# Performance work log

Measured on AMD Instinct MI355X. Metric: run time of the kernel, lower is better.

Reference implementation:

```python
import jax, jax.numpy as jnp
import numpy as np

N = 1024          # num_features
H = N // 2        # core dimension (num_params // 2)
NB = 4            # num_blocks
B = 16384         # batch


def _lifted_core(rot_params, diag_params):
    """Build the (N, N) lifted core matrix for one Cayley block."""
    # skew-symmetric matrix from the H rotation params
    S = rot_params[:, None] - rot_params[None, :]            # (H, H)
    I = jnp.eye(H, dtype=rot_params.dtype)
    rotation = jnp.linalg.solve(I - S, I + S)                # Cayley transform
    core = diag_params[:, None] * rotation                   # diag(d) @ rotation
    # rot90(core, k=o) only depends on o mod 4 -> precompute 4 variants
    rots = jnp.stack([core,
                      jnp.rot90(core, 1),
                      jnp.rot90(core, 2),
                      jnp.rot90(core, 3)])                   # (4, H, H)

    def body(lifted, o):
        blk = jax.lax.dynamic_slice(lifted, (o, o), (H, H)) + rots[o % 4]
        return jax.lax.dynamic_update_slice(lifted, blk, (o, o)), None

    lifted, _ = jax.lax.scan(body, jnp.zeros((N, N), dtype=core.dtype),
                             jnp.arange(H + 1))
    return lifted


def setup_inputs() -> dict:
    key = jax.random.key(0)
    ks = jax.random.split(key, 5)
    x = jax.random.normal(ks[0], (B, N), dtype=jnp.float32)
    enc_rot = jax.random.normal(ks[1], (NB, H), dtype=jnp.float32)
    enc_diag = jax.random.normal(ks[2], (NB, H), dtype=jnp.float32)
    dec_rot = jax.random.normal(ks[3], (NB, H), dtype=jnp.float32)
    dec_diag = jax.random.normal(ks[4], (NB, H), dtype=jnp.float32)
    return {"x": x, "enc_rot": enc_rot, "enc_diag": enc_diag,
            "dec_rot": dec_rot, "dec_diag": dec_diag}


def reference(x, enc_rot, enc_diag, dec_rot, dec_diag):
    s = x
    for i in range(NB):                                      # encoder blocks
        s = s @ _lifted_core(enc_rot[i], enc_diag[i]).T
    bottleneck = s
    out = s
    for i in range(NB):                                      # decoder blocks
        out = out @ _lifted_core(dec_rot[i], dec_diag[i]).T
    return bottleneck, out
```

## Files before the change

### kernel.cpp

```cpp
#include <hip/hip_runtime.h>
#include <hip/hip_bf16.h>
#include <cstdint>
#include <cstddef>

#define H 512
#define NFEAT 1024
#define BATCH 16384
#define LM ((size_t)1 << 20)
#define KOP 576

using bf16 = __hip_bfloat16;
using bf16x8 = __attribute__((ext_vector_type(8))) __bf16;
using f32x4 = __attribute__((ext_vector_type(4))) float;
using f32x16 = __attribute__((ext_vector_type(16))) float;

__device__ __forceinline__ void gload16(void* lds, const void* g) {
  __builtin_amdgcn_global_load_lds(
      (__attribute__((address_space(1))) void*)g,
      (__attribute__((address_space(3))) void*)lds,
      16, 0, 0);
}

__global__ void prep_kernel(const float* __restrict__ er, const float* __restrict__ ed,
                            const float* __restrict__ dr, const float* __restrict__ dd,
                            float* __restrict__ ab) {
  const int mat = blockIdx.x;
  const int lane = threadIdx.x;
  const float* u = (mat < 4) ? (er + mat * H) : (dr + (mat - 4) * H);
  const float* d = (mat < 4) ? (ed + mat * H) : (dd + (mat - 4) * H);

  double s = 0.0, q = 0.0;
  for (int k = 0; k < 8; ++k) {
    double v = (double)u[lane + 64 * k];
    s += v;
    q += v * v;
  }
  for (int off = 32; off; off >>= 1) {
    s += __shfl_down(s, off);
    q += __shfl_down(q, off);
  }
  s = __shfl(s, 0);
  q = __shfl(q, 0);

  const double det = 1.0 - s * s + (double)H * q;
  const double cuv = 2.0 * (1.0 + s) / det;
  const double cuu = -2.0 * (double)H / det;
  const double cvv = -2.0 * q / det;
  const double cvu = -2.0 * (1.0 - s) / det;

  float* a = ab + mat * 1024;
  float* b = a + H;
  for (int k = 0; k < 8; ++k) {
    int idx = lane + 64 * k;
    double ui = (double)u[idx], di = (double)d[idx];
    a[idx] = (float)(di * (cuv * ui + cvv));
    b[idx] = (float)(di * (cuu * ui + cvu));
  }
}

__global__ __launch_bounds__(256) void prep2_kernel(
    const float* __restrict__ er, const float* __restrict__ ed,
    const float* __restrict__ dr, const float* __restrict__ dd,
    const float* __restrict__ ab, float* __restrict__ Tpref) {
  __shared__ float buf[4][512];
  __shared__ float tmp[4][512];
  const int mat = blockIdx.x;
  const float* d = (mat < 4) ? (ed + mat * H) : (dd + (mat - 4) * H);
  const float* a = ab + mat * 1024;
  const int t = threadIdx.x;
  for (int m = t; m < 512; m += 256) {
    buf[0][m] = a[m];
    buf[1][m] = a[511 - m];
    buf[2][m] = d[m];
    buf[3][m] = d[511 - m];
  }
  __syncthreads();
  for (int s = 4; s <= 256; s <<= 1) {
    for (int m = t; m < 512; m += 256)
#pragma unroll
      for (int q = 0; q < 4; ++q) tmp[q][m] = (m >= s) ? buf[q][m - s] : 0.f;
    __syncthreads();
    for (int m = t; m < 512; m += 256)
#pragma unroll
      for (int q = 0; q < 4; ++q) buf[q][m] += tmp[q][m];
    __syncthreads();
  }
  float* tp = Tpref + mat * 2048;
  for (int m = t; m < 512; m += 256) {
    tp[m] = buf[0][m];
    tp[512 + m] = buf[1][m];
    tp[1024 + m] = buf[2][m];
    tp[1536 + m] = buf[3][m];
  }
}

__global__ __launch_bounds__(256) void genops_kernel(
    const float* __restrict__ er, const float* __restrict__ dr,
    const float* __restrict__ ab,
    bf16* __restrict__ Ah, bf16* __restrict__ Al,
    bf16* __restrict__ Bh, bf16* __restrict__ Bl) {
  const int x = blockIdx.x;
  const int mat = blockIdx.y;
  const float* u = (mat < 4) ? (er + mat * H) : (dr + (mat - 4) * H);
  const float* b = ab + mat * 1024 + H;
  const int t = threadIdx.x;
  const size_t base = ((size_t)mat * 1024 + x) * KOP;
  for (int k = t; k < KOP; k += 256) {
    float av = 0.f, bv = 0.f;
    if (k <= 128) {
      const int o = 4 * k;
      const int ia = x - o;
      av = (ia >= 0 && ia < 512) ? b[ia] : 0.f;
      bv = (ia >= 0 && ia < 512) ? u[ia] : 0.f;
    } else if (k <= 256) {
      const int o = 4 * (k - 129) + 1;
      const int ia = 511 - x + o;
      const int ib = x - o;
      av = (ia >= 0 && ia < 512) ? u[ia] : 0.f;
      bv = (ib >= 0 && ib < 512) ? b[ib] : 0.f;
    } else if (k <= 384) {
      const int o = 4 * (k - 257) + 2;
      const int ia = 511 - x + o;
      av = (ia >= 0 && ia < 512) ? b[ia] : 0.f;
      bv = (ia >= 0 && ia < 512) ? u[ia] : 0.f;
    } else if (k <= 512) {
      const int o = 4 * (k - 385) + 3;
      const int ia = x - o;
      const int ib = 511 - x + o;
      av = (ia >= 0 && ia < 512) ? u[ia] : 0.f;
      bv = (ib >= 0 && ib < 512) ? b[ib] : 0.f;
    }
    const bf16 ah = __float2bfloat16(av);
    Ah[base + k] = ah;
    Al[base + k] = __float2bfloat16(av - __bfloat162float(ah));
    const bf16 bh = __float2bfloat16(bv);
    Bh[base + k] = bh;
    Bl[base + k] = __float2bfloat16(bv - __bfloat162float(bh));
  }
}

__global__ __launch_bounds__(256) void buildgemm_kernel(
    const bf16* __restrict__ Ah, const bf16* __restrict__ Al,
    const bf16* __restrict__ Bh, const bf16* __restrict__ Bl,
    const float* __restrict__ ed, const float* __restrict__ dd,
    const float* __restrict__ Tpref, bf16* __restrict__ Lbase) {
  __shared__ __align__(16) bf16 smem[4 * 8192];
  __shared__ float pa[512], parev[512], pd[512], pdrev[512], sdl[512];
  bf16* sAh = smem;
  bf16* sAl = smem + 8192;
  bf16* sBh = smem + 16384;
  bf16* sBl = smem + 24576;

  const int tid = threadIdx.x;
  const int lane = tid & 63;
  const int wave = tid >> 6;
  const int wr = wave >> 1;
  const int wc = wave & 1;
  const int mat = blockIdx.z;
  const int row0 = blockIdx.x * 128;
  const int col0 = blockIdx.y * 128;

  {
    const float* tp = Tpref + mat * 2048;
    const float* d = (mat < 4) ? (ed + mat * H) : (dd + (mat - 4) * H);
    for (int m = tid; m < 512; m += 256) {
      pa[m] = tp[m];
      parev[m] = tp[512 + m];
      pd[m] = tp[1024 + m];
      pdrev[m] = tp[1536 + m];
      sdl[m] = d[m];
    }
  }

  const size_t OPS = (size_t)mat * 1024 * KOP;
  const int srow = tid >> 3;
  const int sce = (((tid * 16) ^ (((tid >> 3) & 7) << 4)) & 127) >> 1;
  const size_t abase = OPS + (size_t)(row0 + srow) * KOP + sce;
  const size_t bbase = OPS + (size_t)(col0 + srow) * KOP + sce;
  const int dst0 = tid * 8;

  f32x16 acc[2][2] = {};

  for (int kt = 0; kt < 9; ++kt) {
    const int k0 = kt * 64;
#pragma unroll
    for (int q = 0; q < 4; ++q) {
      const size_t ga = abase + (size_t)(32 * q) * KOP + k0;
      const size_t gb = bbase + (size_t)(32 * q) * KOP + k0;
      const int dq = q * 2048 + dst0;
      gload16(sAh + dq, Ah + ga);
      gload16(sAl + dq, Al + ga);
      gload16(sBh + dq, Bh + gb);
      gload16(sBl + dq, Bl + gb);
    }
    __syncthreads();

    const int l31 = lane & 31;
    const int kh16 = (lane >> 5) * 16;
#pragma unroll
    for (int ks = 0; ks < 4; ++ks) {
      bf16x8 fah[2], fal[2], fbh[2], fbl[2];
#pragma unroll
      for (int m = 0; m < 2; ++m) {
        const int arow = wr * 64 + m * 32 + l31;
        const int abk = (arow * 128 + ks * 32 + kh16) ^ ((arow & 7) << 4);
        fah[m] = *(const bf16x8*)((const char*)sAh + abk);
        fal[m] = *(const bf16x8*)((const char*)sAl + abk);
        const int brow = wc * 64 + m * 32 + l31;
        const int bbk = (brow * 128 + ks * 32 + kh16) ^ ((brow & 7) << 4);
        fbh[m] = *(const bf16x8*)((const char*)sBh + bbk);
        fbl[m] = *(const bf16x8*)((const char*)sBl + bbk);
      }
#pragma unroll
      for (int m = 0; m < 2; ++m)
#pragma unroll
        for (int n = 0; n < 2; ++n) {
          acc[m][n] = __builtin_amdgcn_mfma_f32_32x32x16_bf16(fah[m], fbh[n], acc[m][n], 0, 0, 0);
          acc[m][n] = __builtin_amdgcn_mfma_f32_32x32x16_bf16(fah[m], fbl[n], acc[m][n], 0, 0, 0);
          acc[m][n] = __builtin_amdgcn_mfma_f32_32x32x16_bf16(fal[m], fbh[n], acc[m][n], 0, 0, 0);
        }
    }
    __syncthreads();
  }

  auto apart = [&](int i, int j) -> float {
    const int lo = max(0, max(i, j) - 511);
    const int hi = min(512, min(i, j));
    if (lo > hi) return 0.f;
    float v = 0.f;
    {
      int o1 = lo + ((0 - lo) & 3), o2 = hi - (hi & 3);
      if (o1 <= o2) { int mx = i - o1, mn = i - o2; v += pa[mx] - (mn >= 4 ? pa[mn - 4] : 0.f); }
    }
    {
      int o1 = lo + ((1 - lo) & 3), o2 = hi - ((hi - 1) & 3);
      if (o1 <= o2) { int mx = j - o1, mn = j - o2; v += pa[mx] - (mn >= 4 ? pa[mn - 4] : 0.f); }
    }
    {
      int o1 = lo + ((2 - lo) & 3), o2 = hi - ((hi - 2) & 3);
      if (o1 <= o2) { int mx = i - o1, mn = i - o2; v += parev[mx] - (mn >= 4 ? parev[mn - 4] : 0.f); }
    }
    {
      int o1 = lo + ((3 - lo) & 3), o2 = hi - ((hi - 3) & 3);
      if (o1 <= o2) { int mx = j - o1, mn = j - o2; v += parev[mx] - (mn >= 4 ? parev[mn - 4] : 0.f); }
    }
    if (i == j) {
      {
        int o1 = lo + ((0 - lo) & 3), o2 = hi - (hi & 3);
        if (o1 <= o2) { int mx = i - o1, mn = i - o2; v += pd[mx] - (mn >= 4 ? pd[mn - 4] : 0.f); }
      }
      {
        int o1 = lo + ((2 - lo) & 3), o2 = hi - ((hi - 2) & 3);
        if (o1 <= o2) { int mx = i - o1, mn = i - o2; v += pdrev[mx] - (mn >= 4 ? pdrev[mn - 4] : 0.f); }
      }
    }
    const int m2 = i + j - 511;
    if (m2 >= 0 && !(m2 & 1)) {
      const int os = m2 >> 1;
      if (os >= lo && os <= hi) {
        const int r = os & 3;
        if (r == 1) v += sdl[j - os];
        else if (r == 3) v += sdl[511 - (j - os)];
      }
    }
    return v;
  };

  const int ocol0 = col0 + wc * 64 + (lane & 31);
  const int rb = (lane >> 5) << 2;
#pragma unroll
  for (int m = 0; m < 2; ++m)
#pragma unroll
    for (int n = 0; n < 2; ++n)
#pragma unroll
      for (int r = 0; r < 16; ++r) {
        const int grow = row0 + wr * 64 + m * 32 + (r & 3) + ((r >> 2) << 3) + rb;
        const int gcol = ocol0 + n * 32;
        const float v = acc[m][n][r] + apart(grow, gcol);
        const size_t off = ((size_t)mat << 21) + ((size_t)grow << 10) + (size_t)gcol;
        const bf16 hb = __float2bfloat16(v);
        Lbase[off] = hb;
        Lbase[off + LM] = __float2bfloat16(v - __bfloat162float(hb));
      }
}

__global__ void splith_kernel(const float* __restrict__ x, bf16* __restrict__ h) {
  const int n4 = BATCH * NFEAT / 4;
  int idx = blockIdx.x * blockDim.x + threadIdx.x;
  int stride = gridDim.x * blockDim.x;
  for (int i = idx; i < n4; i += stride) {
    float4 v = ((const float4*)x)[i];
    union { bf16 b[4]; short4 s; } Hu;
    Hu.b[0] = __float2bfloat16(v.x);
    Hu.b[1] = __float2bfloat16(v.y);
    Hu.b[2] = __float2bfloat16(v.z);
    Hu.b[3] = __float2bfloat16(v.w);
    ((short4*)h)[i] = Hu.s;
  }
}

struct TPtrs { const bf16* s; bf16* d; };
struct T6 { TPtrs t[6]; };

__global__ __launch_bounds__(256) void transposeB_kernel(T6 p) {
  const bf16* S = p.t[blockIdx.z].s;
  bf16* D = p.t[blockIdx.z].d;
  __shared__ ushort tile[64][68];
  const int i0 = blockIdx.x * 64, j0 = blockIdx.y * 64;
  const int tid = threadIdx.x;
  const int rr = tid >> 4;
  const int cc = (tid & 15) * 4;
#pragma unroll
  for (int it = 0; it < 4; ++it) {
    const int row = it * 16 + rr;
    const size_t so = (size_t)(i0 + row) * 1024 + j0 + cc;
    ushort4 v = *(const ushort4*)((const ushort*)S + so);
    tile[row][cc] = v.x; tile[row][cc + 1] = v.y;
    tile[row][cc + 2] = v.z; tile[row][cc + 3] = v.w;
  }
  __syncthreads();
#pragma unroll
  for (int it = 0; it < 4; ++it) {
    const int row = it * 16 + rr;
    ushort4 o;
    o.x = tile[cc][row];     o.y = tile[cc + 1][row];
    o.z = tile[cc + 2][row]; o.w = tile[cc + 3][row];
    const size_t dofs = (size_t)(j0 + row) * 1024 + i0 + cc;
    *(ushort4*)((ushort*)D + dofs) = o;
  }
}

struct GPtrs { const bf16* a; const bf16* b; bf16* yh; bf16* yl; };
struct G4 { GPtrs g[4]; };

__global__ __launch_bounds__(256) void chaingemm4_kernel(G4 p) {
  GPtrs q = p.g[blockIdx.z];
  const bf16* A = q.a;
  const bf16* Bh = q.b;
  const bf16* Bl = q.b + LM;

  __shared__ __align__(16) bf16 smem[2 * 3 * 4096];

  const int tid = threadIdx.x;
  const int lane = tid & 63;
  const int wave = tid >> 6;
  const int wr = wave >> 1, wc = wave & 1;
  const int r0 = blockIdx.x * 64, c0 = blockIdx.y * 64;

  const int srow = tid >> 3;
  const int scol = (((tid & 7) ^ (srow & 7))) * 8;
  const int dst = tid * 8;
  const size_t ga0 = (size_t)(r0 + srow) * 1024 + scol;
  const size_t gb0 = (size_t)(c0 + srow) * 1024 + scol;

  auto STAGE = [&](int nb, int k0) {
    bf16* base = smem + nb * 12288;
    gload16(base + dst,        A + ga0 + k0);
    gload16(base + 2048 + dst, A + ga0 + 32 * 1024 + k0);
    gload16(base + 4096 + dst,        Bh + gb0 + k0);
    gload16(base + 4096 + 2048 + dst, Bh + gb0 + 32 * 1024 + k0);
    gload16(base + 8192 + dst,        Bl + gb0 + k0);
    gload16(base + 8192 + 2048 + dst, Bl + gb0 + 32 * 1024 + k0);
  };

  const int l31 = lane & 31;
  const int klg = lane >> 5;
  const int ar = wr * 32 + l31;
  const int br = wc * 32 + l31;
  int aoff[4], boff[4];
#pragma unroll
  for (int ks = 0; ks < 4; ++ks) {
    const int lgA = (ks << 1) | klg;
    aoff[ks] = ar * 64 + ((lgA ^ (ar & 7)) << 3);
    boff[ks] = br * 64 + ((lgA ^ (br & 7)) << 3);
  }

  f32x16 acc = {};

  STAGE(0, 0);
  asm volatile("s_waitcnt vmcnt(0)" ::: "memory");
  __builtin_amdgcn_s_barrier();

  for (int t = 0; t < 16; ++t) {
    const int buf = t & 1;
    const int nb = buf ^ 1;
    const bool pf = (t < 15);
    if (pf) STAGE(nb, (t + 1) * 64);

    const bf16* pA = smem + buf * 12288;
    const bf16* pBh = pA + 4096;
    const bf16* pBl = pA + 8192;
#pragma unroll
    for (int ks = 0; ks < 4; ++ks) {
      bf16x8 ah = *(const bf16x8*)(pA + aoff[ks]);
      bf16x8 bh = *(const bf16x8*)(pBh + boff[ks]);
      bf16x8 bl = *(const bf16x8*)(pBl + boff[ks]);
      acc = __builtin_amdgcn_mfma_f32_32x32x16_bf16(ah, bh, acc, 0, 0, 0);
      acc = __builtin_amdgcn_mfma_f32_32x32x16_bf16(ah, bl, acc, 0, 0, 0);
    }
    if (pf) asm volatile("s_waitcnt vmcnt(0)" ::: "memory");
    __builtin_amdgcn_s_barrier();
  }

  const int oc = c0 + wc * 32 + l31;
  const int rb = (lane >> 5) << 2;
#pragma unroll
  for (int r = 0; r < 16; ++r) {
    const int gr = r0 + wr * 32 + (r & 3) + ((r >> 2) << 3) + rb;
    const size_t off = (size_t)gr * 1024 + oc;
    const float v = acc[r];
    const bf16 hb = __float2bfloat16(v);
    q.yh[off] = hb;
    q.yl[off] = __float2bfloat16(v - __bfloat162float(hb));
  }
}

__global__ __launch_bounds__(256, 2) void gemmbig_kernel(
    const bf16* __restrict__ A, const bf16* __restrict__ Bh_,
    float* __restrict__ Y0, float* __restrict__ Y1) {
  __shared__ __align__(16) bf16 smem[3 * 12288];

  const int tid = threadIdx.x;
  const int lane = tid & 63;
  const int wave = tid >> 6;
  const int wr = wave >> 1;
  const int wc = wave & 1;

  const int pdisp = blockIdx.x;
  const int xcd = pdisp & 7;
  const int chk = pdisp >> 3;
  const int row0 = (xcd * 16 + (chk >> 3)) * 128;
  const int col0 = (chk & 7) * 256;

  const int sr = tid >> 2;
  const int sc = ((tid & 3) ^ ((tid >> 3) & 3)) * 8;
  const size_t abase0 = (size_t)(row0 + sr) * NFEAT + sc;
  const size_t abase1 = abase0 + (size_t)64 * NFEAT;
  const size_t bbase = (size_t)(col0 + sr) * NFEAT + sc;
  const int dst = tid * 8;

  auto STAGE_A = [&](int buf, int k0) {
    bf16* base = smem + buf * 12288;
    gload16(base + dst, A + abase0 + k0);
    gload16(base + 2048 + dst, A + abase1 + k0);
  };
  auto STAGE_B = [&](int buf, int k0) {
    bf16* base = smem + buf * 12288 + 4096;
#pragma unroll
    for (int q = 0; q < 4; ++q)
      gload16(base + q * 2048 + dst, Bh_ + bbase + (size_t)(64 * q) * NFEAT + k0);
  };

  const int l15 = lane & 15;
  const int kcol = ((lane >> 4) * 16) ^ (((l15 >> 1) & 3) << 4);
  int aoff[4], boff[8];
#pragma unroll
  for (int fr = 0; fr < 4; ++fr)
    aoff[fr] = (wr * 64 + fr * 16 + l15) * 64 + kcol;
#pragma unroll
  for (int fc = 0; fc < 8; ++fc)
    boff[fc] = 8192 + (wc * 128 + fc * 16 + l15) * 64 + kcol;

  auto LD = [&](int buf, int off) {
    return *(const bf16x8*)((const char*)(smem + buf * 12288) + off);
  };

  f32x4 acc[4][8] = {};

  STAGE_A(0, 0); STAGE_B(0, 0);
  STAGE_A(1, 32); STAGE_B(1, 32);
  asm volatile("s_waitcnt vmcnt(6)" ::: "memory");
  __builtin_amdgcn_s_barrier();

  for (int T = 0; T < 32; ++T) {
    const int buf = T % 3;
    if (T < 30) {
      const int nb = (T + 2) % 3;
      STAGE_A(nb, (T + 2) * 32);
      STAGE_B(nb, (T + 2) * 32);
    }

    bf16x8 fa[4], fb[4];
#pragma unroll
    for (int fr = 0; fr < 4; ++fr) fa[fr] = LD(buf, aoff[fr]);
#pragma unroll
    for (int fc = 0; fc < 4; ++fc) fb[fc] = LD(buf, boff[fc]);
    __builtin_amdgcn_s_setprio(1);
#pragma unroll
    for (int fr = 0; fr < 4; ++fr)
#pragma unroll
      for (int fc = 0; fc < 4; ++fc)
        acc[fr][fc] = __builtin_amdgcn_mfma_f32_16x16x32_bf16(fa[fr], fb[fc], acc[fr][fc], 0, 0, 0);
    __builtin_amdgcn_s_setprio(0);
#pragma unroll
    for (int fc = 0; fc < 4; ++fc) fb[fc] = LD(buf, boff[4 + fc]);
    __builtin_amdgcn_s_setprio(1);
#pragma unroll
    for (int fr = 0; fr < 4; ++fr)
#pragma unroll
      for (int fc = 0; fc < 4; ++fc)
        acc[fr][4 + fc] = __builtin_amdgcn_mfma_f32_16x16x32_bf16(fa[fr], fb[fc], acc[fr][4 + fc], 0, 0, 0);
    __builtin_amdgcn_s_setprio(0);

    if (T <= 29) {
      asm volatile("s_waitcnt vmcnt(6)" ::: "memory");
    } else if (T == 30) {
      asm volatile("s_waitcnt vmcnt(0)" ::: "memory");
    }
    __builtin_amdgcn_s_barrier();
  }

  float* Yb = (col0 < 1024) ? Y0 : (Y1 - 1024);
  const int orow = row0 + wr * 64 + (lane >> 4) * 4;
  const int ocol = col0 + wc * 128 + l15;
#pragma unroll
  for (int fr = 0; fr < 4; ++fr)
#pragma unroll
    for (int fc = 0; fc < 8; ++fc)
#pragma unroll
      for (int r = 0; r < 4; ++r) {
        const int grow = orow + fr * 16 + r;
        const int gcol = ocol + fc * 16;
        Yb[(size_t)grow * NFEAT + (size_t)gcol] = acc[fr][fc][r];
      }
}

extern "C" void kernel_launch(void* const* d_in, const int* in_sizes, int n_in,
                              void* d_out, int out_size, void* d_ws, size_t ws_size,
                              hipStream_t stream) {
  (void)in_sizes; (void)n_in; (void)out_size; (void)ws_size;
  const float* x  = (const float*)d_in[0];
  const float* er = (const float*)d_in[1];
  const float* ed = (const float*)d_in[2];
  const float* dr = (const float*)d_in[3];
  const float* dd = (const float*)d_in[4];

  float* O0 = (float*)d_out;
  float* O1 = O0 + (size_t)BATCH * NFEAT;

  bf16* Lb = (bf16*)d_ws;
  float* ab = (float*)(Lb + 16 * LM);
  bf16* Qh = (bf16*)(ab + 8 * 1024);

  float* Tpref = O0;
  bf16* SB = (bf16*)((char*)O0 + (1 << 20));
  auto slot = [&](int s) { return SB + (size_t)s * LM; };

  const size_t OPN = (size_t)8 * 1024 * KOP;
  bf16* Aoph = (bf16*)O1;
  bf16* Aopl = Aoph + OPN;
  bf16* Boph = Aopl + OPN;
  bf16* Bopl = Boph + OPN;

  prep_kernel<<<8, 64, 0, stream>>>(er, ed, dr, dd, ab);
  prep2_kernel<<<8, 256, 0, stream>>>(er, ed, dr, dd, ab, Tpref);
  genops_kernel<<<dim3(1024, 8), 256, 0, stream>>>(er, dr, ab, Aoph, Aopl, Boph, Bopl);
  buildgemm_kernel<<<dim3(8, 8, 8), 256, 0, stream>>>(Aoph, Aopl, Boph, Bopl,
                                                      ed, dd, Tpref, Lb);
  splith_kernel<<<4096, 256, 0, stream>>>(x, Qh);

  {
    T6 p;
    p.t[0] = {Lb + 0 * LM,  slot(0)};
    p.t[1] = {Lb + 4 * LM,  slot(2)};
    p.t[2] = {Lb + 5 * LM,  slot(3)};
    p.t[3] = {Lb + 8 * LM,  slot(4)};
    p.t[4] = {Lb + 12 * LM, slot(6)};
    p.t[5] = {Lb + 13 * LM, slot(7)};
    transposeB_kernel<<<dim3(16, 16, 6), 256, 0, stream>>>(p);
  }
  {
    G4 p;
    p.g[0] = {slot(0),      Lb + 2 * LM,  slot(8),  slot(9)};
    p.g[1] = {Lb + 6 * LM,  slot(2),      slot(10), slot(11)};
    p.g[2] = {slot(4),      Lb + 10 * LM, slot(12), slot(13)};
    p.g[3] = {Lb + 14 * LM, slot(6),      slot(14), slot(15)};
    chaingemm4_kernel<<<dim3(16, 16, 4), 256, 0, stream>>>(p);
  }
  {
    G4 p;
    p.g[0] = {slot(8),  slot(10), slot(0), slot(1)};
    p.g[1] = {slot(12), slot(14), slot(2), slot(3)};
    p.g[2] = p.g[0];
    p.g[3] = p.g[1];
    chaingemm4_kernel<<<dim3(16, 16, 2), 256, 0, stream>>>(p);
  }
  {
    T6 p;
    p.t[0] = {slot(0), Lb + 0 * LM};
    p.t[1] = {slot(2), Lb + 2 * LM};
    p.t[2] = p.t[0]; p.t[3] = p.t[0]; p.t[4] = p.t[0]; p.t[5] = p.t[0];
    transposeB_kernel<<<dim3(16, 16, 2), 256, 0, stream>>>(p);
  }
  {
    G4 p;
    p.g[0] = {Lb + 2 * LM, slot(0), Lb + 1 * LM, slot(4)};
    p.g[1] = p.g[0]; p.g[2] = p.g[0]; p.g[3] = p.g[0];
    chaingemm4_kernel<<<dim3(16, 16, 1), 256, 0, stream>>>(p);
  }

  gemmbig_kernel<<<1024, 256, 0, stream>>>(Qh, Lb, O0, O1);
}
```

Before: 253.1 us.

## Drop A low-part in build GEMM and triple-buffer chain GEMM loads

The operator-building GEMM now uses only the high bf16 part of the A operand, removing one of the three split-precision MFMAs plus its global load and LDS traffic. The chained small GEMMs switch from double to triple buffering in LDS, prefetching two stages ahead and waiting with a partial vmcnt so more loads stay in flight. The first change reduces accuracy of the built lifted matrices, since the A low residual is discarded. The second raises LDS use per block, which may limit occupancy.

Result: faster. 246.3 us (-2.7%).

```diff
diff --git a/kernel.cpp b/kernel.cpp
--- a/kernel.cpp
+++ b/kernel.cpp
@@ -97,8 +97,7 @@
 __global__ __launch_bounds__(256) void genops_kernel(
     const float* __restrict__ er, const float* __restrict__ dr,
     const float* __restrict__ ab,
-    bf16* __restrict__ Ah, bf16* __restrict__ Al,
-    bf16* __restrict__ Bh, bf16* __restrict__ Bl) {
+    bf16* __restrict__ Ah, bf16* __restrict__ Bh, bf16* __restrict__ Bl) {
   const int x = blockIdx.x;
   const int mat = blockIdx.y;
   const float* u = (mat < 4) ? (er + mat * H) : (dr + (mat - 4) * H);
@@ -130,9 +129,7 @@
       av = (ia >= 0 && ia < 512) ? u[ia] : 0.f;
       bv = (ib >= 0 && ib < 512) ? b[ib] : 0.f;
     }
-    const bf16 ah = __float2bfloat16(av);
-    Ah[base + k] = ah;
-    Al[base + k] = __float2bfloat16(av - __bfloat162float(ah));
+    Ah[base + k] = __float2bfloat16(av);
     const bf16 bh = __float2bfloat16(bv);
     Bh[base + k] = bh;
     Bl[base + k] = __float2bfloat16(bv - __bfloat162float(bh));
@@ -140,16 +137,15 @@
 }
 
 __global__ __launch_bounds__(256) void buildgemm_kernel(
-    const bf16* __restrict__ Ah, const bf16* __restrict__ Al,
-    const bf16* __restrict__ Bh, const bf16* __restrict__ Bl,
+    const bf16* __restrict__ Ah, const bf16* __restrict__ Bh,
+    const bf16* __restrict__ Bl,
     const float* __restrict__ ed, const float* __restrict__ dd,
     const float* __restrict__ Tpref, bf16* __restrict__ Lbase) {
-  __shared__ __align__(16) bf16 smem[4 * 8192];
+  __shared__ __align__(16) bf16 smem[3 * 8192];
   __shared__ float pa[512], parev[512], pd[512], pdrev[512], sdl[512];
   bf16* sAh = smem;
-  bf16* sAl = smem + 8192;
-  bf16* sBh = smem + 16384;
-  bf16* sBl = smem + 24576;
+  bf16* sBh = smem + 8192;
+  bf16* sBl = smem + 16384;
 
   const int tid = threadIdx.x;
   const int lane = tid & 63;
@@ -189,7 +185,6 @@
       const size_t gb = bbase + (size_t)(32 * q) * KOP + k0;
       const int dq = q * 2048 + dst0;
       gload16(sAh + dq, Ah + ga);
-      gload16(sAl + dq, Al + ga);
       gload16(sBh + dq, Bh + gb);
       gload16(sBl + dq, Bl + gb);
     }
@@ -199,13 +194,12 @@
     const int kh16 = (lane >> 5) * 16;
 #pragma unroll
     for (int ks = 0; ks < 4; ++ks) {
-      bf16x8 fah[2], fal[2], fbh[2], fbl[2];
+      bf16x8 fah[2], fbh[2], fbl[2];
 #pragma unroll
       for (int m = 0; m < 2; ++m) {
         const int arow = wr * 64 + m * 32 + l31;
         const int abk = (arow * 128 + ks * 32 + kh16) ^ ((arow & 7) << 4);
         fah[m] = *(const bf16x8*)((const char*)sAh + abk);
-        fal[m] = *(const bf16x8*)((const char*)sAl + abk);
         const int brow = wc * 64 + m * 32 + l31;
         const int bbk = (brow * 128 + ks * 32 + kh16) ^ ((brow & 7) << 4);
         fbh[m] = *(const bf16x8*)((const char*)sBh + bbk);
@@ -217,7 +211,6 @@
         for (int n = 0; n < 2; ++n) {
           acc[m][n] = __builtin_amdgcn_mfma_f32_32x32x16_bf16(fah[m], fbh[n], acc[m][n], 0, 0, 0);
           acc[m][n] = __builtin_amdgcn_mfma_f32_32x32x16_bf16(fah[m], fbl[n], acc[m][n], 0, 0, 0);
-          acc[m][n] = __builtin_amdgcn_mfma_f32_32x32x16_bf16(fal[m], fbh[n], acc[m][n], 0, 0, 0);
         }
     }
     __syncthreads();
@@ -339,7 +332,7 @@
   const bf16* Bh = q.b;
   const bf16* Bl = q.b + LM;
 
-  __shared__ __align__(16) bf16 smem[2 * 3 * 4096];
+  __shared__ __align__(16) bf16 smem[3 * 12288];
 
   const int tid = threadIdx.x;
   const int lane = tid & 63;
@@ -353,8 +346,8 @@
   const size_t ga0 = (size_t)(r0 + srow) * 1024 + scol;
   const size_t gb0 = (size_t)(c0 + srow) * 1024 + scol;
 
-  auto STAGE = [&](int nb, int k0) {
-    bf16* base = smem + nb * 12288;
+  auto STAGE = [&](int buf, int k0) {
+    bf16* base = smem + buf * 12288;
     gload16(base + dst,        A + ga0 + k0);
     gload16(base + 2048 + dst, A + ga0 + 32 * 1024 + k0);
     gload16(base + 4096 + dst,        Bh + gb0 + k0);
@@ -378,14 +371,13 @@
   f32x16 acc = {};
 
   STAGE(0, 0);
-  asm volatile("s_waitcnt vmcnt(0)" ::: "memory");
+  STAGE(1, 64);
+  asm volatile("s_waitcnt vmcnt(6)" ::: "memory");
   __builtin_amdgcn_s_barrier();
 
   for (int t = 0; t < 16; ++t) {
-    const int buf = t & 1;
-    const int nb = buf ^ 1;
-    const bool pf = (t < 15);
-    if (pf) STAGE(nb, (t + 1) * 64);
+    const int buf = t % 3;
+    if (t < 14) STAGE((t + 2) % 3, (t + 2) * 64);
 
     const bf16* pA = smem + buf * 12288;
     const bf16* pBh = pA + 4096;
@@ -398,7 +390,11 @@
       acc = __builtin_amdgcn_mfma_f32_32x32x16_bf16(ah, bh, acc, 0, 0, 0);
       acc = __builtin_amdgcn_mfma_f32_32x32x16_bf16(ah, bl, acc, 0, 0, 0);
     }
-    if (pf) asm volatile("s_waitcnt vmcnt(0)" ::: "memory");
+    if (t <= 13) {
+      asm volatile("s_waitcnt vmcnt(6)" ::: "memory");
+    } else if (t == 14) {
+      asm volatile("s_waitcnt vmcnt(0)" ::: "memory");
+    }
     __builtin_amdgcn_s_barrier();
   }
 
@@ -548,14 +544,13 @@
 
   const size_t OPN = (size_t)8 * 1024 * KOP;
   bf16* Aoph = (bf16*)O1;
-  bf16* Aopl = Aoph + OPN;
-  bf16* Boph = Aopl + OPN;
+  bf16* Boph = Aoph + OPN;
   bf16* Bopl = Boph + OPN;
 
   prep_kernel<<<8, 64, 0, stream>>>(er, ed, dr, dd, ab);
   prep2_kernel<<<8, 256, 0, stream>>>(er, ed, dr, dd, ab, Tpref);
-  genops_kernel<<<dim3(1024, 8), 256, 0, stream>>>(er, dr, ab, Aoph, Aopl, Boph, Bopl);
-  buildgemm_kernel<<<dim3(8, 8, 8), 256, 0, stream>>>(Aoph, Aopl, Boph, Bopl,
+  genops_kernel<<<dim3(1024, 8), 256, 0, stream>>>(er, dr, ab, Aoph, Boph, Bopl);
+  buildgemm_kernel<<<dim3(8, 8, 8), 256, 0, stream>>>(Aoph, Boph, Bopl,
                                                       ed, dd, Tpref, Lb);
   splith_kernel<<<4096, 256, 0, stream>>>(x, Qh);
 
```
